# Optimization experiments

Hardware: AMD Instinct MI355X
Metric: run time of the kernel (lower is better)

Reference implementation:

```python
import jax, jax.numpy as jnp
import numpy as np

N, F_IN, F_OUT = 2048, 128, 64


def setup_inputs() -> dict:
    key = jax.random.key(0)
    k0, k1, k2, k3, k4 = jax.random.split(key, 5)
    node_features = jax.random.normal(k0, (N, F_IN), dtype=jnp.float32)
    adjacency_matrix = jax.random.uniform(k1, (N, N), dtype=jnp.float32)
    mask_father = jax.random.uniform(k2, (N, N), dtype=jnp.float32)
    mask_hadamard = jax.random.uniform(k3, (N, N), dtype=jnp.float32)
    # kaiming_uniform (fan_in, relu): bound = sqrt(6 / fan_in) * sqrt(2) adjustment -> gain*sqrt(3/fan_in)
    bound = np.sqrt(2.0) * np.sqrt(3.0 / F_IN)
    weight = jax.random.uniform(k4, (F_IN, F_OUT), dtype=jnp.float32, minval=-bound, maxval=bound)
    bias = jnp.zeros((F_OUT,), dtype=jnp.float32)
    return {
        "node_features": node_features,
        "adjacency_matrix": adjacency_matrix,
        "mask_father": mask_father,
        "mask_hadamard": mask_hadamard,
        "weight": weight,
        "bias": bias,
    }


def reference(node_features, adjacency_matrix, mask_father, mask_hadamard, weight, bias):
    # H[i,f] = (X @ W + b)[i,f]
    H = node_features @ weight + bias  # [N, F]
    # Original math: out[j,f] = sum_k mf[j,k] * H[k,f] * (sum_i A[j,i] * H[i,f] * mh[i,k])
    # G[j,f,k] corresponds to the (masked hadamard @ adjacency) intermediate [N, F, N]
    G = jnp.einsum('ji,if,ik->jfk', adjacency_matrix, H, mask_hadamard)
    out = jnp.einsum('jfk,kf,jk->jf', G, H, mask_father)
    return out
```

## Files before the change

kernel.cpp:

```cpp
#include <hip/hip_runtime.h>
#include <hip/hip_bf16.h>


typedef __attribute__((ext_vector_type(8))) _Float16 f16x8;
typedef __attribute__((ext_vector_type(4))) _Float16 f16x4;
typedef __attribute__((ext_vector_type(4))) float f32x4;

#define N 2048
#define FOUT 64
#define FIN 128
#define NIT 512

__device__ __forceinline__ void gl_lds16(const _Float16* g, _Float16* l) {
    __builtin_amdgcn_global_load_lds(
        (const __attribute__((address_space(1))) void*)g,
        (__attribute__((address_space(3))) void*)l, 16, 0, 0);
}


__global__ __launch_bounds__(256) void k_h(const float* __restrict__ X,
                                           const float* __restrict__ W,
                                           const float* __restrict__ bias,
                                           float* __restrict__ HT,
                                           _Float16* __restrict__ HTh) {
    __shared__ float Ws[FIN * FOUT];
    __shared__ float Xs[4 * FIN];
    int t = threadIdx.x;
#pragma unroll
    for (int s = 0; s < 32; ++s) Ws[t + 256 * s] = W[t + 256 * s];
    int i0 = blockIdx.x * 4;
#pragma unroll
    for (int s = 0; s < 2; ++s) { int idx = t + 256 * s; Xs[idx] = X[(size_t)i0 * FIN + idx]; }
    __syncthreads();
    int f = t & 63, il = t >> 6;
    float h = bias[f];
#pragma unroll
    for (int p = 0; p < FIN; ++p) h = fmaf(Xs[il * FIN + p], Ws[p * FOUT + f], h);
    int i = i0 + il;
    HT[f * N + i] = h;
    HTh[f * N + i] = (_Float16)h;
}

__global__ __launch_bounds__(256) void k_a2h(const float* __restrict__ A,
                                             _Float16* __restrict__ Ah) {
    int g = blockIdx.x * 256 + threadIdx.x;
    float4 v = ((const float4*)A)[g];
    f16x4 o;
    o[0] = (_Float16)v.x; o[1] = (_Float16)v.y; o[2] = (_Float16)v.z; o[3] = (_Float16)v.w;
    ((f16x4*)Ah)[g] = o;
}

__global__ __launch_bounds__(256) void k_mht(const float* __restrict__ mh,
                                             _Float16* __restrict__ mhT) {
    __shared__ float tile[64][65];
    int t = threadIdx.x;
    int bx = blockIdx.x & 31;
    int by = blockIdx.x >> 5;
#pragma unroll
    for (int s = 0; s < 16; ++s) {
        int lin = t + 256 * s;
        int r = lin >> 6, c = lin & 63;
        tile[r][c] = mh[(size_t)(by * 64 + r) * N + bx * 64 + c];
    }
    __syncthreads();
#pragma unroll
    for (int s = 0; s < 16; ++s) {
        int lin = t + 256 * s;
        int kr = lin >> 6, ic = lin & 63;
        mhT[(size_t)(bx * 64 + kr) * N + by * 64 + ic] = (_Float16)tile[ic][kr];
    }
}


#define ISSUE(it_, la_, lb_)                                                  \
    {                                                                         \
        int itc_ = ((it_) < NIT) ? (it_) : (NIT - 1);                         \
        int ib_ = (itc_ & 31) << 6;                                           \
        const _Float16* pa_ = Ah + aoff + ib_;                                \
        const _Float16* pb_ = mhT + boff + (size_t)((itc_ >> 5) << 7) * N + ib_; \
        _Pragma("unroll") for (int c_ = 0; c_ < 4; ++c_) {                    \
            gl_lds16(pa_ + c_ * 8 * N, (la_) + c_ * 512);                     \
            gl_lds16(pb_ + c_ * 8 * N, (lb_) + c_ * 512);                     \
        }                                                                     \
    }

#define COMPUTE(it_, ta_, tb_)                                                \
    {                                                                         \
        int ibb_ = ((it_) & 31) << 6;                                         \
        _Pragma("unroll") for (int s = 0; s < 2; ++s) {                       \
            f16x8 ar_[4], br_[4];                                             \
            _Pragma("unroll") for (int x = 0; x < 4; ++x)                     \
                ar_[x] = *(const f16x8*)&(ta_)[(wj + x * 16 + l16) * 64 +     \
                                               (((q + 4 * s) ^ (l16 & 7)) << 3)]; \
            _Pragma("unroll") for (int x = 0; x < 4; ++x)                     \
                br_[x] = *(const f16x8*)&(tb_)[(wk + x * 16 + l16) * 64 +     \
                                               (((q + 4 * s) ^ (l16 & 7)) << 3)]; \
            f16x8 h0_ = *(const f16x8*)&hbuf[0][ibb_ + s * 32 + (q << 3)];    \
            f16x8 h1_ = *(const f16x8*)&hbuf[1][ibb_ + s * 32 + (q << 3)];    \
            _Pragma("unroll") for (int jj = 0; jj < 4; ++jj) {                \
                f16x8 a0_ = ar_[jj] * h0_;                                    \
                f16x8 a1_ = ar_[jj] * h1_;                                    \
                _Pragma("unroll") for (int kk = 0; kk < 4; ++kk) {            \
                    acc[0][jj][kk] = __builtin_amdgcn_mfma_f32_16x16x32_f16(  \
                        a0_, br_[kk], acc[0][jj][kk], 0, 0, 0);               \
                    acc[1][jj][kk] = __builtin_amdgcn_mfma_f32_16x16x32_f16(  \
                        a1_, br_[kk], acc[1][jj][kk], 0, 0, 0);               \
                }                                                             \
            }                                                                 \
        }                                                                     \
    }

#define EPILOGUE(kt_)                                                         \
    {                                                                         \
        int kbase_ = (kt_) << 7;                                              \
        _Pragma("unroll") for (int jj = 0; jj < 4; ++jj) {                    \
            float t0_[4] = {0.f, 0.f, 0.f, 0.f};                              \
            float t1_[4] = {0.f, 0.f, 0.f, 0.f};                              \
            _Pragma("unroll") for (int kk = 0; kk < 4; ++kk) {                \
                int kg_ = kbase_ + wk + kk * 16 + l16;                        \
                float hk0_ = HT[f0 * N + kg_];                                \
                float hk1_ = HT[(f0 + 1) * N + kg_];                          \
                int jrow_ = jbase + wj + jj * 16 + q * 4;                     \
                _Pragma("unroll") for (int r = 0; r < 4; ++r) {               \
                    float m_ = mf[(size_t)(jrow_ + r) * N + kg_];             \
                    t0_[r] = fmaf(acc[0][jj][kk][r], m_ * hk0_, t0_[r]);      \
                    t1_[r] = fmaf(acc[1][jj][kk][r], m_ * hk1_, t1_[r]);      \
                }                                                             \
            }                                                                 \
            _Pragma("unroll") for (int r = 0; r < 4; ++r) {                   \
                float v0_ = t0_[r], v1_ = t1_[r];                             \
                v0_ += __shfl_xor(v0_, 1); v1_ += __shfl_xor(v1_, 1);         \
                v0_ += __shfl_xor(v0_, 2); v1_ += __shfl_xor(v1_, 2);         \
                v0_ += __shfl_xor(v0_, 4); v1_ += __shfl_xor(v1_, 4);         \
                v0_ += __shfl_xor(v0_, 8); v1_ += __shfl_xor(v1_, 8);         \
                outp[0][jj][r] += v0_;                                        \
                outp[1][jj][r] += v1_;                                        \
            }                                                                 \
        }                                                                     \
        _Pragma("unroll") for (int a_ = 0; a_ < 2; ++a_)                      \
            _Pragma("unroll") for (int b_ = 0; b_ < 4; ++b_)                  \
                _Pragma("unroll") for (int c2_ = 0; c2_ < 4; ++c2_)           \
                    acc[a_][b_][c2_] = (f32x4){0.f, 0.f, 0.f, 0.f};           \
    }

#define SYNC_VM8()                                                            \
    __builtin_amdgcn_sched_barrier(0);                                        \
    __builtin_amdgcn_s_waitcnt(0x0F78);          \
    __builtin_amdgcn_s_barrier();                                             \
    __builtin_amdgcn_sched_barrier(0);

#define SYNC_BARE()                                                           \
    __builtin_amdgcn_sched_barrier(0);                                        \
    __builtin_amdgcn_s_barrier();                                             \
    __builtin_amdgcn_sched_barrier(0);

__global__ __launch_bounds__(256, 2) void k_main(const float* __restrict__ mf,
                                                 const float* __restrict__ HT,
                                                 const _Float16* __restrict__ HTh,
                                                 const _Float16* __restrict__ Ah,
                                                 const _Float16* __restrict__ mhT,
                                                 float* __restrict__ out) {
    __shared__ _Float16 tiles[2][2][128 * 64];
    __shared__ _Float16 hbuf[2][N];
    __shared__ float red[2][4][64];

    int t = threadIdx.x;
    int jbase = (blockIdx.x >> 5) << 7;
    int f0 = (blockIdx.x & 31) << 1;
    int w = t >> 6, lane = t & 63, q = lane >> 4, l16 = lane & 15;
    int wj = (w & 1) << 6, wk = (w >> 1) << 6;

#pragma unroll
    for (int s = 0; s < 2; ++s) {
        int idx = t + 256 * s;
        ((f16x8*)hbuf)[idx] = *(const f16x8*)&HTh[(size_t)(f0 + (idx >> 8)) * N + (idx & 255) * 8];
    }
    __syncthreads();

    int lrow = lane >> 3;
    int lchunk = (lane & 7) ^ lrow;
    size_t aoff = (size_t)(jbase + w * 32 + lrow) * N + lchunk * 8;
    size_t boff = (size_t)(w * 32 + lrow) * N + lchunk * 8;
    _Float16* la0 = &tiles[0][0][w * 2048];
    _Float16* lb0 = &tiles[0][1][w * 2048];
    _Float16* la1 = &tiles[1][0][w * 2048];
    _Float16* lb1 = &tiles[1][1][w * 2048];
    const _Float16* ta0 = &tiles[0][0][0];
    const _Float16* tb0 = &tiles[0][1][0];
    const _Float16* ta1 = &tiles[1][0][0];
    const _Float16* tb1 = &tiles[1][1][0];

    float outp[2][4][4];
    f32x4 acc[2][4][4];
#pragma unroll
    for (int a = 0; a < 2; ++a)
#pragma unroll
        for (int b = 0; b < 4; ++b)
#pragma unroll
            for (int c = 0; c < 4; ++c) {
                outp[a][b][c] = 0.f;
                acc[a][b][c] = (f32x4){0.f, 0.f, 0.f, 0.f};
            }

    ISSUE(0, la0, lb0);
    ISSUE(1, la1, lb1);

#pragma unroll 1
    for (int it2 = 0; it2 < NIT; it2 += 2) {
        SYNC_VM8();
        COMPUTE(it2, ta0, tb0);
        SYNC_BARE();
        ISSUE(it2 + 2, la0, lb0);

        SYNC_VM8();
        COMPUTE(it2 + 1, ta1, tb1);
        SYNC_BARE();
        ISSUE(it2 + 3, la1, lb1);
        if (((it2 + 1) & 31) == 31) { EPILOGUE((it2 + 1) >> 5); }
    }

    __syncthreads();
    if (l16 == 0) {
#pragma unroll
        for (int fi = 0; fi < 2; ++fi)
#pragma unroll
            for (int jj = 0; jj < 4; ++jj)
#pragma unroll
                for (int r = 0; r < 4; ++r)
                    red[fi][w][jj * 16 + q * 4 + r] = outp[fi][jj][r];
    }
    __syncthreads();
    if (t < 128) {
        int j = t;
#pragma unroll
        for (int fi = 0; fi < 2; ++fi) {
            float v = (j < 64) ? (red[fi][0][j] + red[fi][2][j])
                               : (red[fi][1][j - 64] + red[fi][3][j - 64]);
            out[(size_t)(jbase + j) * FOUT + f0 + fi] = v;
        }
    }
}

extern "C" void kernel_launch(void* const* d_in, const int* in_sizes, int n_in,
                              void* d_out, int out_size, void* d_ws, size_t ws_size,
                              hipStream_t stream) {
    const float* X    = (const float*)d_in[0];
    const float* A    = (const float*)d_in[1];
    const float* mf   = (const float*)d_in[2];
    const float* mh   = (const float*)d_in[3];
    const float* W    = (const float*)d_in[4];
    const float* bias = (const float*)d_in[5];
    float* out = (float*)d_out;

    float*    HT  = (float*)d_ws;
    _Float16* HTh = (_Float16*)((char*)d_ws + 524288);
    _Float16* Ah  = (_Float16*)((char*)d_ws + 1048576);
    _Float16* mhT = (_Float16*)((char*)d_ws + 1048576 + 8388608);

    k_h<<<N / 4, 256, 0, stream>>>(X, W, bias, HT, HTh);
    k_a2h<<<(N * N / 4) / 256, 256, 0, stream>>>(A, Ah);
    k_mht<<<(N / 64) * (N / 64), 256, 0, stream>>>(mh, mhT);
    k_main<<<16 * 32, 256, 0, stream>>>(mf, HT, HTh, Ah, mhT, out);
}
```

Measured before the change: 1.062 ms.

## Restructure main loop to one barrier per stage with interleaved MFMA scheduling

The double-buffered main loop now uses a single __syncthreads per stage. The next tile's global-to-LDS load is issued right after the barrier and before the current tile's compute, replacing the earlier two-ahead prefetch with partial vmcnt waits. COMPUTE loads both k-halves up front and adds sched_group_barrier hints to interleave LDS reads with MFMAs. The per-thread output partials move from registers into the shared `red` buffer to lower register pressure. The trade-off is a shorter prefetch distance and full memory waits at each barrier.

```diff
diff --git a/kernel.cpp b/kernel.cpp
--- a/kernel.cpp
+++ b/kernel.cpp
@@ -87,27 +87,50 @@
 #define COMPUTE(it_, ta_, tb_)                                                \
     {                                                                         \
         int ibb_ = ((it_) & 31) << 6;                                         \
-        _Pragma("unroll") for (int s = 0; s < 2; ++s) {                       \
-            f16x8 ar_[4], br_[4];                                             \
-            _Pragma("unroll") for (int x = 0; x < 4; ++x)                     \
-                ar_[x] = *(const f16x8*)&(ta_)[(wj + x * 16 + l16) * 64 +     \
-                                               (((q + 4 * s) ^ (l16 & 7)) << 3)]; \
-            _Pragma("unroll") for (int x = 0; x < 4; ++x)                     \
-                br_[x] = *(const f16x8*)&(tb_)[(wk + x * 16 + l16) * 64 +     \
-                                               (((q + 4 * s) ^ (l16 & 7)) << 3)]; \
-            f16x8 h0_ = *(const f16x8*)&hbuf[0][ibb_ + s * 32 + (q << 3)];    \
-            f16x8 h1_ = *(const f16x8*)&hbuf[1][ibb_ + s * 32 + (q << 3)];    \
-            _Pragma("unroll") for (int jj = 0; jj < 4; ++jj) {                \
-                f16x8 a0_ = ar_[jj] * h0_;                                    \
-                f16x8 a1_ = ar_[jj] * h1_;                                    \
-                _Pragma("unroll") for (int kk = 0; kk < 4; ++kk) {            \
-                    acc[0][jj][kk] = __builtin_amdgcn_mfma_f32_16x16x32_f16(  \
-                        a0_, br_[kk], acc[0][jj][kk], 0, 0, 0);               \
-                    acc[1][jj][kk] = __builtin_amdgcn_mfma_f32_16x16x32_f16(  \
-                        a1_, br_[kk], acc[1][jj][kk], 0, 0, 0);               \
-                }                                                             \
-            }                                                                 \
-        }                                                                     \
+        f16x8 h00_ = *(const f16x8*)&hbuf[0][ibb_ + (q << 3)];                \
+        f16x8 h01_ = *(const f16x8*)&hbuf[1][ibb_ + (q << 3)];                \
+        f16x8 ar0_[4], br0_[4];                                               \
+        _Pragma("unroll") for (int x = 0; x < 4; ++x) {                       \
+            ar0_[x] = *(const f16x8*)&(ta_)[(wj + x * 16 + l16) * 64 +        \
+                                            ((q ^ (l16 & 7)) << 3)];          \
+            br0_[x] = *(const f16x8*)&(tb_)[(wk + x * 16 + l16) * 64 +        \
+                                            ((q ^ (l16 & 7)) << 3)];          \
+        }                                                                     \
+        f16x8 h10_ = *(const f16x8*)&hbuf[0][ibb_ + 32 + (q << 3)];           \
+        f16x8 h11_ = *(const f16x8*)&hbuf[1][ibb_ + 32 + (q << 3)];           \
+        f16x8 ar1_[4], br1_[4];                                               \
+        _Pragma("unroll") for (int x = 0; x < 4; ++x) {                       \
+            ar1_[x] = *(const f16x8*)&(ta_)[(wj + x * 16 + l16) * 64 +        \
+                                            (((q + 4) ^ (l16 & 7)) << 3)];    \
+            br1_[x] = *(const f16x8*)&(tb_)[(wk + x * 16 + l16) * 64 +        \
+                                            (((q + 4) ^ (l16 & 7)) << 3)];    \
+        }                                                                     \
+        _Pragma("unroll") for (int jj = 0; jj < 4; ++jj) {                    \
+            f16x8 a00_ = ar0_[jj] * h00_;                                     \
+            f16x8 a01_ = ar0_[jj] * h01_;                                     \
+            _Pragma("unroll") for (int kk = 0; kk < 4; ++kk) {                \
+                acc[0][jj][kk] = __builtin_amdgcn_mfma_f32_16x16x32_f16(      \
+                    a00_, br0_[kk], acc[0][jj][kk], 0, 0, 0);                 \
+                acc[1][jj][kk] = __builtin_amdgcn_mfma_f32_16x16x32_f16(      \
+                    a01_, br0_[kk], acc[1][jj][kk], 0, 0, 0);                 \
+            }                                                                 \
+        }                                                                     \
+        _Pragma("unroll") for (int jj = 0; jj < 4; ++jj) {                    \
+            f16x8 a10_ = ar1_[jj] * h10_;                                     \
+            f16x8 a11_ = ar1_[jj] * h11_;                                     \
+            _Pragma("unroll") for (int kk = 0; kk < 4; ++kk) {                \
+                acc[0][jj][kk] = __builtin_amdgcn_mfma_f32_16x16x32_f16(      \
+                    a10_, br1_[kk], acc[0][jj][kk], 0, 0, 0);                 \
+                acc[1][jj][kk] = __builtin_amdgcn_mfma_f32_16x16x32_f16(      \
+                    a11_, br1_[kk], acc[1][jj][kk], 0, 0, 0);                 \
+            }                                                                 \
+        }                                                                     \
+        __builtin_amdgcn_sched_group_barrier(0x100, 10, 0);      \
+        __builtin_amdgcn_sched_group_barrier(0x008, 16, 0);     \
+        __builtin_amdgcn_sched_group_barrier(0x100,  5, 0);      \
+        __builtin_amdgcn_sched_group_barrier(0x008,  8, 0);     \
+        __builtin_amdgcn_sched_group_barrier(0x100,  5, 0);      \
+        __builtin_amdgcn_sched_group_barrier(0x008, 40, 0);     \
     }
 
 #define EPILOGUE(kt_)                                                         \
@@ -133,8 +156,10 @@
                 v0_ += __shfl_xor(v0_, 2); v1_ += __shfl_xor(v1_, 2);         \
                 v0_ += __shfl_xor(v0_, 4); v1_ += __shfl_xor(v1_, 4);         \
                 v0_ += __shfl_xor(v0_, 8); v1_ += __shfl_xor(v1_, 8);         \
-                outp[0][jj][r] += v0_;                                        \
-                outp[1][jj][r] += v1_;                                        \
+                if (l16 == 0) {                                               \
+                    red[0][w][jj * 16 + (q << 2) + r] += v0_;                 \
+                    red[1][w][jj * 16 + (q << 2) + r] += v1_;                 \
+                }                                                             \
             }                                                                 \
         }                                                                     \
         _Pragma("unroll") for (int a_ = 0; a_ < 2; ++a_)                      \
@@ -142,17 +167,6 @@
                 _Pragma("unroll") for (int c2_ = 0; c2_ < 4; ++c2_)           \
                     acc[a_][b_][c2_] = (f32x4){0.f, 0.f, 0.f, 0.f};           \
     }
-
-#define SYNC_VM8()                                                            \
-    __builtin_amdgcn_sched_barrier(0);                                        \
-    __builtin_amdgcn_s_waitcnt(0x0F78);          \
-    __builtin_amdgcn_s_barrier();                                             \
-    __builtin_amdgcn_sched_barrier(0);
-
-#define SYNC_BARE()                                                           \
-    __builtin_amdgcn_sched_barrier(0);                                        \
-    __builtin_amdgcn_s_barrier();                                             \
-    __builtin_amdgcn_sched_barrier(0);
 
 __global__ __launch_bounds__(256, 2) void k_main(const float* __restrict__ mf,
                                                  const float* __restrict__ HT,
@@ -174,6 +188,7 @@
     for (int s = 0; s < 2; ++s) {
         int idx = t + 256 * s;
         ((f16x8*)hbuf)[idx] = *(const f16x8*)&HTh[(size_t)(f0 + (idx >> 8)) * N + (idx & 255) * 8];
+        ((float*)red)[idx] = 0.f;
     }
     __syncthreads();
 
@@ -190,45 +205,28 @@
     const _Float16* ta1 = &tiles[1][0][0];
     const _Float16* tb1 = &tiles[1][1][0];
 
-    float outp[2][4][4];
     f32x4 acc[2][4][4];
 #pragma unroll
     for (int a = 0; a < 2; ++a)
 #pragma unroll
         for (int b = 0; b < 4; ++b)
 #pragma unroll
-            for (int c = 0; c < 4; ++c) {
-                outp[a][b][c] = 0.f;
-                acc[a][b][c] = (f32x4){0.f, 0.f, 0.f, 0.f};
-            }
+            for (int c = 0; c < 4; ++c) acc[a][b][c] = (f32x4){0.f, 0.f, 0.f, 0.f};
 
     ISSUE(0, la0, lb0);
-    ISSUE(1, la1, lb1);
 
 #pragma unroll 1
     for (int it2 = 0; it2 < NIT; it2 += 2) {
-        SYNC_VM8();
+        __syncthreads();
+        ISSUE(it2 + 1, la1, lb1);
         COMPUTE(it2, ta0, tb0);
-        SYNC_BARE();
+
+        __syncthreads();
         ISSUE(it2 + 2, la0, lb0);
-
-        SYNC_VM8();
         COMPUTE(it2 + 1, ta1, tb1);
-        SYNC_BARE();
-        ISSUE(it2 + 3, la1, lb1);
         if (((it2 + 1) & 31) == 31) { EPILOGUE((it2 + 1) >> 5); }
     }
 
-    __syncthreads();
-    if (l16 == 0) {
-#pragma unroll
-        for (int fi = 0; fi < 2; ++fi)
-#pragma unroll
-            for (int jj = 0; jj < 4; ++jj)
-#pragma unroll
-                for (int r = 0; r < 4; ++r)
-                    red[fi][w][jj * 16 + q * 4 + r] = outp[fi][jj][r];
-    }
     __syncthreads();
     if (t < 128) {
         int j = t;
```

Measured after the change: 1.042 ms. Within noise of the previous version (-1.9%).
